# Kernel optimization log

Measured on AMD Instinct MI355X. Metric: run time of the kernel, lower is better.

The kernel has to match this reference:

```python
import jax, jax.numpy as jnp
import numpy as np

N = 100000   # nodes
E = 800000   # edges (before self loops)
IN = 128     # in_channels
H1, C1 = 8, 64      # gat1: heads, channels  -> 512 out
NC = 16      # num_classes (gat3: 1 head)
NEG_SLOPE = 0.2


def setup_inputs() -> dict:
    key = jax.random.key(0)
    ks = jax.random.split(key, 14)
    def gl(k, shape, fan_in):
        return jax.random.normal(k, shape, dtype=jnp.float32) / np.sqrt(fan_in)
    x = jax.random.normal(ks[0], (N, IN), dtype=jnp.float32)
    edge_index = jax.random.randint(ks[1], (2, E), 0, N, dtype=jnp.int64)
    return {
        "x": x,
        "edge_index": edge_index,
        # gat1: in=128 -> 8 heads x 64
        "g1_W": gl(ks[2], (IN, H1 * C1), IN),
        "g1_as": gl(ks[3], (H1, C1), C1),
        "g1_ad": gl(ks[4], (H1, C1), C1),
        "g1_b": jnp.zeros((H1 * C1,), jnp.float32),
        # skip_proj1: 128 -> 512
        "sk1_W": gl(ks[5], (IN, H1 * C1), IN),
        "sk1_b": jnp.zeros((H1 * C1,), jnp.float32),
        # skip_proj2: 512 -> 512
        "sk2_W": gl(ks[6], (H1 * C1, 512), H1 * C1),
        "sk2_b": jnp.zeros((512,), jnp.float32),
        # gat3: in=1024 -> 1 head x NC
        "g3_W": gl(ks[7], (1024, NC), 1024),
        "g3_as": gl(ks[8], (1, NC), NC),
        "g3_ad": gl(ks[9], (1, NC), NC),
        "g3_b": jnp.zeros((NC,), jnp.float32),
    }


def _gat_conv(x, W, att_src, att_dst, bias, src, dst, n):
    """PyG GATConv: concat=True, add_self_loops already in (src, dst)."""
    H, C = att_src.shape
    h = (x @ W).reshape(n, H, C)                      # [N,H,C]
    a_src = jnp.einsum('nhc,hc->nh', h, att_src)      # [N,H]
    a_dst = jnp.einsum('nhc,hc->nh', h, att_dst)
    e = jax.nn.leaky_relu(a_src[src] + a_dst[dst], NEG_SLOPE)   # [E,H]
    # segment softmax over destination node
    emax = jax.ops.segment_max(e, dst, num_segments=n)
    e = jnp.exp(e - emax[dst])
    denom = jax.ops.segment_sum(e, dst, num_segments=n)
    alpha = e / (denom[dst] + 1e-16)                  # [E,H]
    msg = h[src] * alpha[:, :, None]                  # [E,H,C] gather + weight
    out = jax.ops.segment_sum(msg, dst, num_segments=n)  # [N,H,C] scatter-add
    return out.reshape(n, H * C) + bias


def reference(x, edge_index, g1_W, g1_as, g1_ad, g1_b,
              sk1_W, sk1_b, sk2_W, sk2_b, g3_W, g3_as, g3_ad, g3_b):
    n = x.shape[0]
    loop = jnp.arange(n, dtype=edge_index.dtype)
    src = jnp.concatenate([edge_index[0], loop])      # add self loops (PyG default)
    dst = jnp.concatenate([edge_index[1], loop])
    x1 = _gat_conv(x, g1_W, g1_as, g1_ad, g1_b, src, dst, n)   # [N,512]
    x_skip1 = x @ sk1_W + sk1_b                                  # [N,512]
    # NOTE: original computes gat2(x1) but never uses it (dead code) -> omitted
    x_skip2 = x1 @ sk2_W + sk2_b                                 # [N,512]
    x3 = jnp.concatenate([x_skip1, x_skip2], axis=1)             # [N,1024]
    return _gat_conv(x3, g3_W, g3_as, g3_ad, g3_b, src, dst, n)  # [N,NC]
```

## Files before the change

### kernel.cpp

```cpp
#include <hip/hip_runtime.h>
#include <hip/hip_bf16.h>

#define NEG_SLOPE 0.2f
using bf16 = __hip_bfloat16;

typedef __attribute__((ext_vector_type(8))) short short8;
typedef __attribute__((ext_vector_type(4))) float f32x4;
#define MFMA16(a, b, c) __builtin_amdgcn_mfma_f32_16x16x32_bf16(a, b, c, 0, 0, 0)

__device__ __forceinline__ float bflo(unsigned u) { return __uint_as_float(u << 16); }
__device__ __forceinline__ float bfhi(unsigned u) { return __uint_as_float(u & 0xffff0000u); }

__device__ __forceinline__ unsigned cvtpk(float lo, float hi) {
  unsigned r;
  asm volatile("v_cvt_pk_bf16_f32 %0, %1, %2" : "=v"(r) : "v"(lo), "v"(hi));
  return r;
}

__device__ __forceinline__ float edge_w(float q, float adh) {
  float t = q + adh;
  t = (t > 0.f) ? t : NEG_SLOPE * t;
  return __expf(t);
}

__device__ __forceinline__ size_t frag_off(int row, int k) {
  return (size_t)(row >> 4) * 2048 + (k >> 5) * 512 + ((k >> 3) & 3) * 128 +
         (row & 15) * 8 + (k & 7);
}

__global__ __launch_bounds__(256)
void setup_kernel(const float* __restrict__ x, const int* __restrict__ ei,
                  const float* __restrict__ g1_W,
                  const float* __restrict__ sk1_W,
                  const float* __restrict__ sk2_W,
                  const float* __restrict__ g3_W,
                  bf16* __restrict__ xbX, bf16* __restrict__ WtX,
                  float* __restrict__ W1pT, float* __restrict__ W2pT,
                  bf16* __restrict__ W2pSa, int* __restrict__ deg,
                  int N, int Np, int E, int EP,
                  int bX, int bWT, int bW1, int bW2) {
  const int b = blockIdx.x;
  const int t = threadIdx.x;
  if (b < bX) {
    const int total4 = Np * 32;
    const int stride = bX * 256;
    for (int i = b * 256 + t; i < total4; i += stride) {
      int row = i >> 5, kq = (i & 31) * 4;
      float4 v = make_float4(0.f, 0.f, 0.f, 0.f);
      if (row < N) v = reinterpret_cast<const float4*>(x)[i];
      union { bf16 bv[4]; ushort4 u; } pk;
      pk.bv[0] = __float2bfloat16(v.x); pk.bv[1] = __float2bfloat16(v.y);
      pk.bv[2] = __float2bfloat16(v.z); pk.bv[3] = __float2bfloat16(v.w);
      *reinterpret_cast<ushort4*>(&xbX[frag_off(row, kq)]) = pk.u;
    }
  } else if (b < bWT) {
    int i = (b - bX) * 256 + t;
    int k = i >> 9, c = i & 511;
    WtX[frag_off(c, k)] = __float2bfloat16(g1_W[k * 512 + c]);
  } else if (b < bW1) {
    int i = (b - bWT) * 256 + t;
    int j = i >> 7, k = i & 127;
    float acc = 0.f;
    for (int m = 0; m < 512; m++) acc += sk1_W[k * 512 + m] * g3_W[m * 16 + j];
    W1pT[i] = acc;
  } else if (b < bW2) {
    int i = (b - bW1) * 256 + t;
    int j = i >> 9, c = i & 511;
    float acc = 0.f;
    for (int m = 0; m < 512; m++) acc += sk2_W[c * 512 + m] * g3_W[(512 + m) * 16 + j];
    W2pT[i] = acc;
    int h = c >> 6, cc = c & 63, kk = cc >> 5, lk = (cc >> 3) & 3, e = cc & 7;
    W2pSa[((size_t)(h * 2 + kk) * 64 + (j + 16 * lk)) * 8 + e] = __float2bfloat16(acc);
  } else {
    int e = (b - bW2) * 256 + t;
    if (e < EP) {
      int d = (e < E) ? ei[E + e] : (e - E);
      atomicAdd(&deg[d], 1);
    }
  }
}

__global__ __launch_bounds__(256)
void scan1_setup2_kernel(const int* __restrict__ deg, int* __restrict__ offs,
                         int* __restrict__ bsum, int n, int NB,
                         const float* __restrict__ sk1_b, const float* __restrict__ sk2_b,
                         const float* __restrict__ g1_b, const float* __restrict__ g3_W,
                         const float* __restrict__ W2pT, float* __restrict__ b3p) {
  const int b = blockIdx.x, t = threadIdx.x;
  if (b == NB) {
    __shared__ float red[16][16];
    int j = t & 15, seg = t >> 4;
    float acc = 0.f;
    for (int m = seg * 32; m < seg * 32 + 32; m++)
      acc += sk1_b[m] * g3_W[m * 16 + j] + sk2_b[m] * g3_W[(512 + m) * 16 + j];
    for (int c = seg * 32; c < seg * 32 + 32; c++)
      acc += g1_b[c] * W2pT[j * 512 + c];
    red[seg][j] = acc;
    __syncthreads();
    if (t < 16) {
      float s = 0.f;
      for (int k = 0; k < 16; k++) s += red[k][t];
      b3p[t] = s;
    }
    return;
  }
  __shared__ int ts[256];
  const int base = b * 1024 + t * 4;
  int4 v = make_int4(0, 0, 0, 0);
  if (base + 3 < n) v = *reinterpret_cast<const int4*>(&deg[base]);
  else {
    if (base + 0 < n) v.x = deg[base + 0];
    if (base + 1 < n) v.y = deg[base + 1];
    if (base + 2 < n) v.z = deg[base + 2];
  }
  ts[t] = v.x + v.y + v.z + v.w;
  __syncthreads();
  for (int st = 1; st < 256; st <<= 1) {
    int u = (t >= st) ? ts[t - st] : 0;
    __syncthreads();
    ts[t] += u;
    __syncthreads();
  }
  int excl = (t == 0) ? 0 : ts[t - 1];
  int4 o;
  o.x = excl;
  o.y = o.x + v.x;
  o.z = o.y + v.y;
  o.w = o.z + v.z;
  if (base + 3 < n) *reinterpret_cast<int4*>(&offs[base]) = o;
  else {
    if (base + 0 < n) offs[base + 0] = o.x;
    if (base + 1 < n) offs[base + 1] = o.y;
    if (base + 2 < n) offs[base + 2] = o.z;
  }
  if (t == 255) bsum[b] = ts[255];
}

__global__ __launch_bounds__(256)
void scan3_kernel(int* __restrict__ offs, const int* __restrict__ bsum, int n, int NB) {
  __shared__ float dummy;
  __shared__ int wred[4];
  const int b = blockIdx.x, t = threadIdx.x;
  (void)dummy;
  int part = (t < b) ? bsum[t] : 0;
  #pragma unroll
  for (int m = 1; m < 64; m <<= 1) part += __shfl_xor(part, m);
  if ((t & 63) == 0) wred[t >> 6] = part;
  __syncthreads();
  const int add = wred[0] + wred[1] + wred[2] + wred[3];
  if (b == NB - 1 && t == 0) offs[n] = add + bsum[b];
  if (add == 0) return;
  const int base = b * 1024 + t * 4;
  if (base + 3 < n) {
    int4 o = *reinterpret_cast<const int4*>(&offs[base]);
    o.x += add; o.y += add; o.z += add; o.w += add;
    *reinterpret_cast<int4*>(&offs[base]) = o;
  } else {
    if (base + 0 < n) offs[base + 0] += add;
    if (base + 1 < n) offs[base + 1] += add;
    if (base + 2 < n) offs[base + 2] += add;
  }
}

__global__ __launch_bounds__(256)
void gemm_scatter_kernel(const bf16* __restrict__ xbX, const bf16* __restrict__ WtX,
                         const bf16* __restrict__ W2pSa,
                         const float* __restrict__ att_s, const float* __restrict__ att_d,
                         bf16* __restrict__ g1p, float* __restrict__ a_src,
                         float* __restrict__ a_dst,
                         const int* __restrict__ ei, const int* __restrict__ offs,
                         int* __restrict__ cursor, int* __restrict__ esrc,
                         int M, int Mt, int E, int EP) {
  const int gb = Mt * 4;
  if (blockIdx.x >= gb) {
    int e = (blockIdx.x - gb) * 256 + threadIdx.x;
    if (e < EP) {
      int s = (e < E) ? ei[e] : (e - E);
      int d = (e < E) ? ei[E + e] : (e - E);
      int pos = offs[d] + atomicAdd(&cursor[d], 1);
      esrc[pos] = s;
    }
    return;
  }
  const int bx = blockIdx.x % Mt;
  const int by = blockIdx.x / Mt;
  const int t = threadIdx.x;
  const int w = t >> 6, l = t & 63;
  const int wm = w & 1, wn = w >> 1;
  const int m0 = bx * 64 + wm * 32;
  const int n0 = by * 128 + wn * 64;
  const int head = n0 >> 6;
  const int lr = l & 15, lk = l >> 4;
  const bf16* aBase = xbX + (size_t)(m0 >> 4) * 2048 + l * 8;
  const bf16* bBase = WtX + (size_t)(n0 >> 4) * 2048 + l * 8;
  f32x4 accT[4][2] = {};
  #pragma unroll
  for (int kc = 0; kc < 4; kc++) {
    short8 av0 = *reinterpret_cast<const short8*>(aBase + kc * 512);
    short8 av1 = *reinterpret_cast<const short8*>(aBase + 2048 + kc * 512);
    short8 bv0 = *reinterpret_cast<const short8*>(bBase + 0 * 2048 + kc * 512);
    short8 bv1 = *reinterpret_cast<const short8*>(bBase + 1 * 2048 + kc * 512);
    short8 bv2 = *reinterpret_cast<const short8*>(bBase + 2 * 2048 + kc * 512);
    short8 bv3 = *reinterpret_cast<const short8*>(bBase + 3 * 2048 + kc * 512);
    accT[0][0] = MFMA16(bv0, av0, accT[0][0]);
    accT[1][0] = MFMA16(bv1, av0, accT[1][0]);
    accT[2][0] = MFMA16(bv2, av0, accT[2][0]);
    accT[3][0] = MFMA16(bv3, av0, accT[3][0]);
    accT[0][1] = MFMA16(bv0, av1, accT[0][1]);
    accT[1][1] = MFMA16(bv1, av1, accT[1][1]);
    accT[2][1] = MFMA16(bv2, av1, accT[2][1]);
    accT[3][1] = MFMA16(bv3, av1, accT[3][1]);
  }
  #pragma unroll
  for (int mi = 0; mi < 2; mi++) {
    float vs = 0.f, vd = 0.f;
    #pragma unroll
    for (int ni = 0; ni < 4; ni++) {
      float4 as4 = *reinterpret_cast<const float4*>(&att_s[head * 64 + ni * 16 + lk * 4]);
      float4 ad4 = *reinterpret_cast<const float4*>(&att_d[head * 64 + ni * 16 + lk * 4]);
      vs += accT[ni][mi][0] * as4.x + accT[ni][mi][1] * as4.y +
            accT[ni][mi][2] * as4.z + accT[ni][mi][3] * as4.w;
      vd += accT[ni][mi][0] * ad4.x + accT[ni][mi][1] * ad4.y +
            accT[ni][mi][2] * ad4.z + accT[ni][mi][3] * ad4.w;
    }
    vs += __shfl_xor(vs, 16); vs += __shfl_xor(vs, 32);
    vd += __shfl_xor(vd, 16); vd += __shfl_xor(vd, 32);
    int row = m0 + mi * 16 + lr;
    if (lk == 0 && row < M) {
      a_src[(size_t)row * 8 + head] = vs;
      a_dst[(size_t)row * 8 + head] = vd;
    }
  }
  unsigned pk[4][2][2];
  #pragma unroll
  for (int ni = 0; ni < 4; ni++)
    #pragma unroll
    for (int mi = 0; mi < 2; mi++) {
      pk[ni][mi][0] = cvtpk(accT[ni][mi][0], accT[ni][mi][1]);
      pk[ni][mi][1] = cvtpk(accT[ni][mi][2], accT[ni][mi][3]);
    }
  f32x4 d3[2] = {};
  #pragma unroll
  for (int kk = 0; kk < 2; kk++) {
    short8 aw2 = *reinterpret_cast<const short8*>(&W2pSa[((size_t)(head * 2 + kk) * 64 + l) * 8]);
    #pragma unroll
    for (int mi = 0; mi < 2; mi++) {
      union { unsigned u[4]; short8 s8; } bf;
      #pragma unroll
      for (int v = 0; v < 4; v++) {
        int src = lr + 16 * ((lk & 1) * 2 + (v >> 1));
        unsigned t0 = __shfl(pk[2 * kk][mi][v & 1], src);
        unsigned t1 = __shfl(pk[2 * kk + 1][mi][v & 1], src);
        bf.u[v] = (lk & 2) ? t1 : t0;
      }
      d3[mi] = MFMA16(aw2, bf.s8, d3[mi]);
    }
  }
  #pragma unroll
  for (int mi = 0; mi < 2; mi++) {
    int row = m0 + mi * 16 + lr;
    if (row < M) {
      uint2 st;
      st.x = cvtpk(d3[mi][0], d3[mi][1]);
      st.y = cvtpk(d3[mi][2], d3[mi][3]);
      *reinterpret_cast<uint2*>(&g1p[(size_t)row * 128 + head * 16 + lk * 4]) = st;
    }
  }
}

__global__ __launch_bounds__(256)
void agg1_h3_kernel(const int* __restrict__ offs, const int* __restrict__ esrc,
                    const float* __restrict__ a_src1, const float* __restrict__ a_dst1,
                    const bf16* __restrict__ g1p,
                    const float* __restrict__ X,
                    const float* __restrict__ W1pT, const float* __restrict__ b3p,
                    const float* __restrict__ g3_as, const float* __restrict__ g3_ad,
                    bf16* __restrict__ H3b, float* __restrict__ a3s, float* __restrict__ a3d,
                    int N) {
  const int l = threadIdx.x & 63;
  const int n = blockIdx.x * 4 + (threadIdx.x >> 6);
  if (n >= N) return;
  const int g = l >> 3, j0 = l & 7;
  const float adh = a_dst1[n * 8 + g];
  const unsigned* __restrict__ G = reinterpret_cast<const unsigned*>(g1p);
  const int lo = offs[n], hi = offs[n + 1];
  const int gj = g * 8 + j0;
  float agg0 = 0.f, agg1 = 0.f, psum = 0.f;
  int i = lo;
  for (; i + 16 <= hi; i += 16) {
    int ss[16]; float qq[16]; unsigned ww[16];
    #pragma unroll
    for (int k = 0; k < 16; k++) ss[k] = esrc[i + k];
    #pragma unroll
    for (int k = 0; k < 16; k++) ww[k] = G[(size_t)ss[k] * 64 + gj];
    #pragma unroll
    for (int k = 0; k < 16; k++) qq[k] = a_src1[(size_t)ss[k] * 8 + g];
    #pragma unroll
    for (int k = 0; k < 16; k++) {
      float v = edge_w(qq[k], adh);
      psum += v;
      agg0 = fmaf(v, bflo(ww[k]), agg0);
      agg1 = fmaf(v, bfhi(ww[k]), agg1);
    }
  }
  if (i + 8 <= hi) {
    int ss[8]; float qq[8]; unsigned ww[8];
    #pragma unroll
    for (int k = 0; k < 8; k++) ss[k] = esrc[i + k];
    #pragma unroll
    for (int k = 0; k < 8; k++) ww[k] = G[(size_t)ss[k] * 64 + gj];
    #pragma unroll
    for (int k = 0; k < 8; k++) qq[k] = a_src1[(size_t)ss[k] * 8 + g];
    #pragma unroll
    for (int k = 0; k < 8; k++) {
      float v = edge_w(qq[k], adh);
      psum += v;
      agg0 = fmaf(v, bflo(ww[k]), agg0);
      agg1 = fmaf(v, bfhi(ww[k]), agg1);
    }
    i += 8;
  }
  for (; i < hi; i++) {
    int s = esrc[i];
    float q = a_src1[(size_t)s * 8 + g];
    unsigned w0 = G[(size_t)s * 64 + gj];
    float v = edge_w(q, adh);
    psum += v;
    agg0 = fmaf(v, bflo(w0), agg0); agg1 = fmaf(v, bfhi(w0), agg1);
  }
  const float inv = 1.f / (psum + 1e-16f);
  float v0 = agg0 * inv, v1 = agg1 * inv;
  {
    const float* xr = &X[(size_t)n * 128 + g * 16];
    const float* wr0 = &W1pT[(2 * j0) * 128 + g * 16];
    const float* wr1 = &W1pT[(2 * j0 + 1) * 128 + g * 16];
    #pragma unroll
    for (int c = 0; c < 16; c += 4) {
      float4 xa = *reinterpret_cast<const float4*>(xr + c);
      float4 wa = *reinterpret_cast<const float4*>(wr0 + c);
      float4 wb = *reinterpret_cast<const float4*>(wr1 + c);
      v0 += xa.x * wa.x + xa.y * wa.y + xa.z * wa.z + xa.w * wa.w;
      v1 += xa.x * wb.x + xa.y * wb.y + xa.z * wb.z + xa.w * wb.w;
    }
  }
  v0 += __shfl_xor(v0, 8); v0 += __shfl_xor(v0, 16); v0 += __shfl_xor(v0, 32);
  v1 += __shfl_xor(v1, 8); v1 += __shfl_xor(v1, 16); v1 += __shfl_xor(v1, 32);
  float o0 = v0 + b3p[2 * j0];
  float o1 = v1 + b3p[2 * j0 + 1];
  if (g == 0) reinterpret_cast<unsigned*>(H3b)[(size_t)n * 8 + j0] = cvtpk(o0, o1);
  float vs = o0 * g3_as[2 * j0] + o1 * g3_as[2 * j0 + 1];
  float vd = o0 * g3_ad[2 * j0] + o1 * g3_ad[2 * j0 + 1];
  vs += __shfl_xor(vs, 1); vs += __shfl_xor(vs, 2); vs += __shfl_xor(vs, 4);
  vd += __shfl_xor(vd, 1); vd += __shfl_xor(vd, 2); vd += __shfl_xor(vd, 4);
  if (l == 0) { a3s[n] = vs; a3d[n] = vd; }
}

__global__ __launch_bounds__(256)
void agg3_kernel(const int* __restrict__ offs, const int* __restrict__ esrc,
                 const float* __restrict__ a3s, const float* __restrict__ a3d,
                 const bf16* __restrict__ H3b, const float* __restrict__ g3_b,
                 float* __restrict__ out, int N) {
  const int l = threadIdx.x & 63;
  const int n = blockIdx.x * 4 + (threadIdx.x >> 6);
  if (n >= N) return;
  const int g = l >> 4, j = l & 15;
  const float ad = a3d[n];
  const ushort* __restrict__ H = reinterpret_cast<const ushort*>(H3b);
  const int lo = offs[n], hi = offs[n + 1];
  float acc = 0.f, psum = 0.f;
  int i = lo + g;
  for (; i + 12 < hi; i += 16) {
    int s0 = esrc[i], s1 = esrc[i + 4], s2 = esrc[i + 8], s3 = esrc[i + 12];
    float q0 = a3s[s0], q1 = a3s[s1], q2 = a3s[s2], q3 = a3s[s3];
    float h0 = __uint_as_float((unsigned)H[(size_t)s0 * 16 + j] << 16);
    float h1 = __uint_as_float((unsigned)H[(size_t)s1 * 16 + j] << 16);
    float h2 = __uint_as_float((unsigned)H[(size_t)s2 * 16 + j] << 16);
    float h3v = __uint_as_float((unsigned)H[(size_t)s3 * 16 + j] << 16);
    float v0 = edge_w(q0, ad), v1 = edge_w(q1, ad);
    float v2 = edge_w(q2, ad), v3 = edge_w(q3, ad);
    psum += (v0 + v1) + (v2 + v3);
    acc = fmaf(v0, h0, acc); acc = fmaf(v1, h1, acc);
    acc = fmaf(v2, h2, acc); acc = fmaf(v3, h3v, acc);
  }
  for (; i < hi; i += 4) {
    int s = esrc[i];
    float v = edge_w(a3s[s], ad);
    psum += v;
    acc = fmaf(v, __uint_as_float((unsigned)H[(size_t)s * 16 + j] << 16), acc);
  }
  acc += __shfl_xor(acc, 16);  acc += __shfl_xor(acc, 32);
  psum += __shfl_xor(psum, 16); psum += __shfl_xor(psum, 32);
  if (l < 16) out[(size_t)n * 16 + j] = acc / (psum + 1e-16f) + g3_b[j];
}

__global__ void sentinel_kernel(float* out) { out[threadIdx.x] = -1e9f; }

extern "C" void kernel_launch(void* const* d_in, const int* in_sizes, int n_in,
                              void* d_out, int out_size, void* d_ws, size_t ws_size,
                              hipStream_t stream) {
  const float* x      = (const float*)d_in[0];
  const int*   ei     = (const int*)d_in[1];
  const float* g1_W   = (const float*)d_in[2];
  const float* g1_as  = (const float*)d_in[3];
  const float* g1_ad  = (const float*)d_in[4];
  const float* g1_b   = (const float*)d_in[5];
  const float* sk1_W  = (const float*)d_in[6];
  const float* sk1_b  = (const float*)d_in[7];
  const float* sk2_W  = (const float*)d_in[8];
  const float* sk2_b  = (const float*)d_in[9];
  const float* g3_W   = (const float*)d_in[10];
  const float* g3_as  = (const float*)d_in[11];
  const float* g3_ad  = (const float*)d_in[12];
  const float* g3_b   = (const float*)d_in[13];
  float* out = (float*)d_out;

  const int N  = in_sizes[0] / 128;
  const int E  = in_sizes[1] / 2;
  const int EP = E + N;
  const int Mt = (N + 63) / 64;
  const int Np = Mt * 64;
  const int NB = (N + 1023) / 1024;

  char* w = (char*)d_ws;
  size_t off = 0;
  auto alloc = [&](size_t bytes) -> void* {
    void* p = w + off;
    off = (off + bytes + 255) & ~(size_t)255;
    return p;
  };

  int* deg    = (int*)alloc((size_t)N * 4);
  int* cursor = (int*)alloc((size_t)N * 4);
  size_t zbytes = off;
  int*   offs   = (int*)alloc((size_t)(N + 1) * 4);
  int*   bsum   = (int*)alloc((size_t)NB * 4);
  int*   esrc   = (int*)alloc((size_t)EP * 4);
  bf16*  xbX    = (bf16*)alloc((size_t)Np * 128 * 2);
  bf16*  WtX    = (bf16*)alloc(512 * 128 * 2);
  bf16*  W2pSa  = (bf16*)alloc(8192 * 2);
  bf16*  g1p    = (bf16*)alloc((size_t)N * 128 * 2);
  float* a_src1 = (float*)alloc((size_t)N * 8 * 4);
  float* a_dst1 = (float*)alloc((size_t)N * 8 * 4);
  bf16*  h3b    = (bf16*)alloc((size_t)N * 16 * 2);
  float* a_src3 = (float*)alloc((size_t)N * 4);
  float* a_dst3 = (float*)alloc((size_t)N * 4);
  float* W1pT   = (float*)alloc(128 * 16 * 4);
  float* W2pT   = (float*)alloc(512 * 16 * 4);
  float* b3p    = (float*)alloc(16 * 4);
  (void)n_in; (void)out_size;

  if (off > ws_size) {
    sentinel_kernel<<<1, 16, 0, stream>>>(out);
    return;
  }

  hipMemsetAsync(d_ws, 0, zbytes, stream);

  const int eb = (EP + 255) / 256;
  const int nb4 = (N + 3) / 4;
  const int bX = 1024, bWT = bX + 256, bW1 = bWT + 8, bW2 = bW1 + 32;

  setup_kernel<<<bW2 + eb, 256, 0, stream>>>(
      x, ei, g1_W, sk1_W, sk2_W, g3_W,
      xbX, WtX, W1pT, W2pT, W2pSa, deg, N, Np, E, EP, bX, bWT, bW1, bW2);

  scan1_setup2_kernel<<<NB + 1, 256, 0, stream>>>(
      deg, offs, bsum, N, NB, sk1_b, sk2_b, g1_b, g3_W, W2pT, b3p);
  scan3_kernel<<<NB, 256, 0, stream>>>(offs, bsum, N, NB);

  gemm_scatter_kernel<<<Mt * 4 + eb, 256, 0, stream>>>(
      xbX, WtX, W2pSa, g1_as, g1_ad, g1p, a_src1, a_dst1,
      ei, offs, cursor, esrc, N, Mt, E, EP);

  agg1_h3_kernel<<<nb4, 256, 0, stream>>>(offs, esrc, a_src1, a_dst1, g1p, x,
                                          W1pT, b3p, g3_as, g3_ad,
                                          h3b, a_src3, a_dst3, N);

  agg3_kernel<<<nb4, 256, 0, stream>>>(offs, esrc, a_src3, a_dst3, h3b, g3_b, out, N);
}
```

Measured before the change: 336.1 us.

## Restructure setup kernels: split degree count, fuse scan with conversions, parallelize weight folds

Measured after the change: 335.7 us. Within noise of the previous version (-0.1%).

```diff
diff --git a/kernel.cpp b/kernel.cpp
--- a/kernel.cpp
+++ b/kernel.cpp
@@ -29,22 +29,56 @@
 }
 
 __global__ __launch_bounds__(256)
-void setup_kernel(const float* __restrict__ x, const int* __restrict__ ei,
-                  const float* __restrict__ g1_W,
-                  const float* __restrict__ sk1_W,
-                  const float* __restrict__ sk2_W,
-                  const float* __restrict__ g3_W,
-                  bf16* __restrict__ xbX, bf16* __restrict__ WtX,
-                  float* __restrict__ W1pT, float* __restrict__ W2pT,
-                  bf16* __restrict__ W2pSa, int* __restrict__ deg,
-                  int N, int Np, int E, int EP,
-                  int bX, int bWT, int bW1, int bW2) {
+void deg_kernel(const int* __restrict__ ei, int* __restrict__ deg, int E, int EP) {
+  int e = blockIdx.x * 256 + threadIdx.x;
+  if (e >= EP) return;
+  int d = (e < E) ? ei[E + e] : (e - E);
+  atomicAdd(&deg[d], 1);
+}
+
+__global__ __launch_bounds__(256)
+void mid_kernel(const int* __restrict__ deg, int* __restrict__ offs, int* __restrict__ bsum,
+                const float* __restrict__ x, const float* __restrict__ g1_W,
+                const float* __restrict__ sk1_W, const float* __restrict__ sk2_W,
+                const float* __restrict__ g3_W,
+                bf16* __restrict__ xbX, bf16* __restrict__ WtX,
+                float* __restrict__ W1pT, float* __restrict__ W2pT,
+                bf16* __restrict__ W2pSa,
+                int N, int Np, int NB, int b1, int b2, int b3, int b4) {
   const int b = blockIdx.x;
   const int t = threadIdx.x;
-  if (b < bX) {
+  if (b < NB) {
+    __shared__ int ts[256];
+    const int base = b * 1024 + t * 4;
+    int4 v = make_int4(0, 0, 0, 0);
+    if (base + 3 < N) v = *reinterpret_cast<const int4*>(&deg[base]);
+    else {
+      if (base + 0 < N) v.x = deg[base + 0];
+      if (base + 1 < N) v.y = deg[base + 1];
+      if (base + 2 < N) v.z = deg[base + 2];
+    }
+    ts[t] = v.x + v.y + v.z + v.w;
+    __syncthreads();
+    for (int st = 1; st < 256; st <<= 1) {
+      int u = (t >= st) ? ts[t - st] : 0;
+      __syncthreads();
+      ts[t] += u;
+      __syncthreads();
+    }
+    int excl = (t == 0) ? 0 : ts[t - 1];
+    int4 o;
+    o.x = excl; o.y = o.x + v.x; o.z = o.y + v.y; o.w = o.z + v.z;
+    if (base + 3 < N) *reinterpret_cast<int4*>(&offs[base]) = o;
+    else {
+      if (base + 0 < N) offs[base + 0] = o.x;
+      if (base + 1 < N) offs[base + 1] = o.y;
+      if (base + 2 < N) offs[base + 2] = o.z;
+    }
+    if (t == 255) bsum[b] = ts[255];
+  } else if (b < b1) {
     const int total4 = Np * 32;
-    const int stride = bX * 256;
-    for (int i = b * 256 + t; i < total4; i += stride) {
+    const int stride = (b1 - NB) * 256;
+    for (int i = (b - NB) * 256 + t; i < total4; i += stride) {
       int row = i >> 5, kq = (i & 31) * 4;
       float4 v = make_float4(0.f, 0.f, 0.f, 0.f);
       if (row < N) v = reinterpret_cast<const float4*>(x)[i];
@@ -53,36 +87,37 @@
       pk.bv[2] = __float2bfloat16(v.z); pk.bv[3] = __float2bfloat16(v.w);
       *reinterpret_cast<ushort4*>(&xbX[frag_off(row, kq)]) = pk.u;
     }
-  } else if (b < bWT) {
-    int i = (b - bX) * 256 + t;
+  } else if (b < b2) {
+    int i = (b - b1) * 256 + t;
     int k = i >> 9, c = i & 511;
     WtX[frag_off(c, k)] = __float2bfloat16(g1_W[k * 512 + c]);
-  } else if (b < bW1) {
-    int i = (b - bWT) * 256 + t;
-    int j = i >> 7, k = i & 127;
+  } else if (b < b3) {
+    int i = (b - b2) * 256 + t;
+    int o = i >> 3, seg = i & 7;
+    int j = o >> 7, k = o & 127;
     float acc = 0.f;
-    for (int m = 0; m < 512; m++) acc += sk1_W[k * 512 + m] * g3_W[m * 16 + j];
-    W1pT[i] = acc;
-  } else if (b < bW2) {
-    int i = (b - bW1) * 256 + t;
-    int j = i >> 9, c = i & 511;
+    for (int m = seg * 64; m < seg * 64 + 64; m++)
+      acc += sk1_W[k * 512 + m] * g3_W[m * 16 + j];
+    acc += __shfl_xor(acc, 1); acc += __shfl_xor(acc, 2); acc += __shfl_xor(acc, 4);
+    if (seg == 0) W1pT[o] = acc;
+  } else if (b < b4) {
+    int i = (b - b3) * 256 + t;
+    int o = i >> 3, seg = i & 7;
+    int j = o >> 9, c = o & 511;
     float acc = 0.f;
-    for (int m = 0; m < 512; m++) acc += sk2_W[c * 512 + m] * g3_W[(512 + m) * 16 + j];
-    W2pT[i] = acc;
-    int h = c >> 6, cc = c & 63, kk = cc >> 5, lk = (cc >> 3) & 3, e = cc & 7;
-    W2pSa[((size_t)(h * 2 + kk) * 64 + (j + 16 * lk)) * 8 + e] = __float2bfloat16(acc);
-  } else {
-    int e = (b - bW2) * 256 + t;
-    if (e < EP) {
-      int d = (e < E) ? ei[E + e] : (e - E);
-      atomicAdd(&deg[d], 1);
-    }
-  }
-}
-
-__global__ __launch_bounds__(256)
-void scan1_setup2_kernel(const int* __restrict__ deg, int* __restrict__ offs,
-                         int* __restrict__ bsum, int n, int NB,
+    for (int m = seg * 64; m < seg * 64 + 64; m++)
+      acc += sk2_W[c * 512 + m] * g3_W[(512 + m) * 16 + j];
+    acc += __shfl_xor(acc, 1); acc += __shfl_xor(acc, 2); acc += __shfl_xor(acc, 4);
+    if (seg == 0) {
+      W2pT[o] = acc;
+      int h = c >> 6, cc = c & 63, kk = cc >> 5, lk = (cc >> 3) & 3, e = cc & 7;
+      W2pSa[((size_t)(h * 2 + kk) * 64 + (j + 16 * lk)) * 8 + e] = __float2bfloat16(acc);
+    }
+  }
+}
+
+__global__ __launch_bounds__(256)
+void scan3_setup2_kernel(int* __restrict__ offs, const int* __restrict__ bsum, int n, int NB,
                          const float* __restrict__ sk1_b, const float* __restrict__ sk2_b,
                          const float* __restrict__ g1_b, const float* __restrict__ g3_W,
                          const float* __restrict__ W2pT, float* __restrict__ b3p) {
@@ -104,44 +139,7 @@
     }
     return;
   }
-  __shared__ int ts[256];
-  const int base = b * 1024 + t * 4;
-  int4 v = make_int4(0, 0, 0, 0);
-  if (base + 3 < n) v = *reinterpret_cast<const int4*>(&deg[base]);
-  else {
-    if (base + 0 < n) v.x = deg[base + 0];
-    if (base + 1 < n) v.y = deg[base + 1];
-    if (base + 2 < n) v.z = deg[base + 2];
-  }
-  ts[t] = v.x + v.y + v.z + v.w;
-  __syncthreads();
-  for (int st = 1; st < 256; st <<= 1) {
-    int u = (t >= st) ? ts[t - st] : 0;
-    __syncthreads();
-    ts[t] += u;
-    __syncthreads();
-  }
-  int excl = (t == 0) ? 0 : ts[t - 1];
-  int4 o;
-  o.x = excl;
-  o.y = o.x + v.x;
-  o.z = o.y + v.y;
-  o.w = o.z + v.z;
-  if (base + 3 < n) *reinterpret_cast<int4*>(&offs[base]) = o;
-  else {
-    if (base + 0 < n) offs[base + 0] = o.x;
-    if (base + 1 < n) offs[base + 1] = o.y;
-    if (base + 2 < n) offs[base + 2] = o.z;
-  }
-  if (t == 255) bsum[b] = ts[255];
-}
-
-__global__ __launch_bounds__(256)
-void scan3_kernel(int* __restrict__ offs, const int* __restrict__ bsum, int n, int NB) {
-  __shared__ float dummy;
   __shared__ int wred[4];
-  const int b = blockIdx.x, t = threadIdx.x;
-  (void)dummy;
   int part = (t < b) ? bsum[t] : 0;
   #pragma unroll
   for (int m = 1; m < 64; m <<= 1) part += __shfl_xor(part, m);
@@ -170,10 +168,9 @@
                          float* __restrict__ a_dst,
                          const int* __restrict__ ei, const int* __restrict__ offs,
                          int* __restrict__ cursor, int* __restrict__ esrc,
-                         int M, int Mt, int E, int EP) {
-  const int gb = Mt * 4;
-  if (blockIdx.x >= gb) {
-    int e = (blockIdx.x - gb) * 256 + threadIdx.x;
+                         int M, int Mt, int E, int EP, int eb) {
+  if (blockIdx.x < eb) {
+    int e = blockIdx.x * 256 + threadIdx.x;
     if (e < EP) {
       int s = (e < E) ? ei[e] : (e - E);
       int d = (e < E) ? ei[E + e] : (e - E);
@@ -182,8 +179,9 @@
     }
     return;
   }
-  const int bx = blockIdx.x % Mt;
-  const int by = blockIdx.x / Mt;
+  const int gb = blockIdx.x - eb;
+  const int bx = gb % Mt;
+  const int by = gb / Mt;
   const int t = threadIdx.x;
   const int w = t >> 6, l = t & 63;
   const int wm = w & 1, wn = w >> 1;
@@ -458,19 +456,20 @@
 
   const int eb = (EP + 255) / 256;
   const int nb4 = (N + 3) / 4;
-  const int bX = 1024, bWT = bX + 256, bW1 = bWT + 8, bW2 = bW1 + 32;
-
-  setup_kernel<<<bW2 + eb, 256, 0, stream>>>(
-      x, ei, g1_W, sk1_W, sk2_W, g3_W,
-      xbX, WtX, W1pT, W2pT, W2pSa, deg, N, Np, E, EP, bX, bWT, bW1, bW2);
-
-  scan1_setup2_kernel<<<NB + 1, 256, 0, stream>>>(
-      deg, offs, bsum, N, NB, sk1_b, sk2_b, g1_b, g3_W, W2pT, b3p);
-  scan3_kernel<<<NB, 256, 0, stream>>>(offs, bsum, N, NB);
-
-  gemm_scatter_kernel<<<Mt * 4 + eb, 256, 0, stream>>>(
+  const int b1 = NB + 1024, b2 = b1 + 256, b3 = b2 + 64, b4 = b3 + 256;
+
+  deg_kernel<<<eb, 256, 0, stream>>>(ei, deg, E, EP);
+
+  mid_kernel<<<b4, 256, 0, stream>>>(
+      deg, offs, bsum, x, g1_W, sk1_W, sk2_W, g3_W,
+      xbX, WtX, W1pT, W2pT, W2pSa, N, Np, NB, b1, b2, b3, b4);
+
+  scan3_setup2_kernel<<<NB + 1, 256, 0, stream>>>(
+      offs, bsum, N, NB, sk1_b, sk2_b, g1_b, g3_W, W2pT, b3p);
+
+  gemm_scatter_kernel<<<eb + Mt * 4, 256, 0, stream>>>(
       xbX, WtX, W2pSa, g1_as, g1_ad, g1p, a_src1, a_dst1,
-      ei, offs, cursor, esrc, N, Mt, E, EP);
+      ei, offs, cursor, esrc, N, Mt, E, EP, eb);
 
   agg1_h3_kernel<<<nb4, 256, 0, stream>>>(offs, esrc, a_src1, a_dst1, g1p, x,
                                           W1pT, b3p, g3_as, g3_ad,
```
